# Kernel optimization log

Measured on AMD Instinct MI355X. Metric: run time of the kernel, lower is better.

## Reference

```python
import jax, jax.numpy as jnp
import numpy as np

E_DIM = 64
N_EMBED = 8192

def setup_inputs() -> dict:
    key = jax.random.key(0)
    k1, k2 = jax.random.split(key)
    x = jax.random.normal(k1, (16, E_DIM, 32, 32), dtype=jnp.float32)   # [B, e_dim, H, W]
    embed = jax.random.normal(k2, (E_DIM, N_EMBED), dtype=jnp.float32)  # codebook [e_dim, n_embed]
    return {"x": x, "embed": embed}

def reference(x, embed):
    e_dim, n_embed = embed.shape
    # NCHW -> NHWC
    xp = jnp.transpose(x, (0, 2, 3, 1))              # [B, H, W, e_dim]
    flat = xp.reshape(-1, e_dim)                     # [N, e_dim]
    # squared-distance expansion: ||f||^2 - 2 f.E + ||e||^2  -> [N, n_embed]
    distance = (jnp.sum(flat * flat, axis=1, keepdims=True)
                - 2.0 * flat @ embed
                + jnp.sum(embed * embed, axis=0, keepdims=True))
    embed_idx = jnp.argmax(-distance, axis=1)        # [N] nearest code ids
    embed_idx = embed_idx.reshape(xp.shape[:-1])     # [B, H, W]
    # gather codes: embedding table is embed.T -> [n_embed, e_dim]
    quantize = jnp.take(embed.T, embed_idx, axis=0)  # [B, H, W, e_dim]
    return quantize
```

## Files before the change

### kernel.cpp

```cpp
#include <hip/hip_runtime.h>


typedef __attribute__((ext_vector_type(8))) __bf16 bf16x8;
typedef __attribute__((ext_vector_type(4))) float f32x4;
typedef unsigned int u32;
typedef unsigned long long u64;

union frag_cast { f32x4 f; bf16x8 b; };
__device__ __forceinline__ bf16x8 as_bf16x8(f32x4 v) { frag_cast u; u.f = v; return u.b; }

#define N_ROWS  16384
#define E_DIM   64
#define N_EMBED 8192
#define NCHUNK  16
#define COLS_PER_BLOCK (N_EMBED / NCHUNK)
#define N_ST (COLS_PER_BLOCK / 64)
#define ROWS_PER_BLOCK 256
#define N_ROWBLK (N_ROWS / ROWS_PER_BLOCK)
#define NT 4
#define MARGIN_THR 2e-3f

#define WS_AH   0u
#define WS_AL   (2u << 20)
#define WS_B    (4u << 20)
#define WS_ET   (6u << 20)
#define WS_BIAS (8u << 20)
#define WS_PB1  (WS_BIAS + (64u << 10))
#define WS_PI1  (WS_PB1 + (1u << 20))
#define WS_PB2  (WS_PI1 + (1u << 20))
#define WS_FIDX (WS_PB2 + (1u << 20))
#define WS_FLAG (WS_FIDX + (64u << 10))
#define WS_CNT  (WS_FLAG + (64u << 10))
#define WS_FKEY (WS_CNT + (4u << 10))

__device__ __forceinline__ u32 f32_key(float s) {
    u32 u = __float_as_uint(s);
    return (u & 0x80000000u) ? ~u : (u | 0x80000000u);
}

__device__ __forceinline__ void async16(const void* g, void* l) {
    __builtin_amdgcn_global_load_lds(
        (const __attribute__((address_space(1))) void*)g,
        (__attribute__((address_space(3))) void*)l, 16, 0, 0);
}

__global__ __launch_bounds__(256) void prep(
        const float* __restrict__ x, const float* __restrict__ embed, char* ws) {
    __shared__ float tile[64][65];
    __bf16* Ah = (__bf16*)(ws + WS_AH);
    __bf16* Al = (__bf16*)(ws + WS_AL);
    float*  eT = (float*)(ws + WS_ET);
    float*  bias = (float*)(ws + WS_BIAS);
    const int t = threadIdx.x;
    const int blk = blockIdx.x;

    if (blk < 256) {
        const int b = blk >> 4, p0 = (blk & 15) * 64;
        {
            const int c = t >> 2, seg = (t & 3) * 16;
            const float* src = x + b * 65536 + c * 1024 + p0 + seg;
#pragma unroll
            for (int i = 0; i < 16; ++i) tile[c][seg + i] = src[i];
        }
        __syncthreads();
        const int p = t >> 2, cq = (t & 3) * 16;
        const long row = b * 1024 + p0 + p;
        bf16x8 vh0, vh1, vl0, vl1;
#pragma unroll
        for (int i = 0; i < 16; ++i) {
            float f = tile[cq + i][p];
            __bf16 h = (__bf16)f;
            __bf16 l = (__bf16)(f - (float)h);
            if (i < 8) { vh0[i] = h; vl0[i] = l; }
            else       { vh1[i - 8] = h; vl1[i - 8] = l; }
        }
        *(bf16x8*)(Ah + row * 64 + cq) = vh0;
        *(bf16x8*)(Ah + row * 64 + cq + 8) = vh1;
        *(bf16x8*)(Al + row * 64 + cq) = vl0;
        *(bf16x8*)(Al + row * 64 + cq + 8) = vl1;
    } else {
        if (blk == 256 && t == 0) *(int*)(ws + WS_CNT) = 0;
        const int g = blk - 256;
        const int jbase = g * 64;
        char* Bg = ws + WS_B + (size_t)g * 16384;
        {
            const int c = t >> 2, seg = (t & 3) * 16;
            const float* src = embed + c * N_EMBED + jbase + seg;
#pragma unroll
            for (int i = 0; i < 16; ++i) tile[c][seg + i] = src[i];
        }
        __syncthreads();
        if (t < 64) {
            float s = 0.f;
#pragma unroll
            for (int c = 0; c < 64; ++c) { float v = tile[c][t]; s = fmaf(v, v, s); }
            bias[jbase + t] = -0.5f * s;
        }
        const int jl = t >> 2, cq = (t & 3) * 16;
        bf16x8 vh0, vh1, vl0, vl1;
#pragma unroll
        for (int i = 0; i < 16; ++i) {
            float f = tile[cq + i][jl];
            eT[(long)(jbase + jl) * 64 + cq + i] = f;
            __bf16 h = (__bf16)f;
            __bf16 l = (__bf16)(f - (float)h);
            if (i < 8) { vh0[i] = h; vl0[i] = l; }
            else       { vh1[i - 8] = h; vl1[i - 8] = l; }
        }
        const int k0 = (cq >> 3), sw = jl & 7;
        __bf16* hi = (__bf16*)Bg + jl * 64;
        __bf16* lo = (__bf16*)(Bg + 8192) + jl * 64;
        *(bf16x8*)(hi + ((k0 ^ sw) * 8))       = vh0;
        *(bf16x8*)(hi + (((k0 + 1) ^ sw) * 8)) = vh1;
        *(bf16x8*)(lo + ((k0 ^ sw) * 8))       = vl0;
        *(bf16x8*)(lo + (((k0 + 1) ^ sw) * 8)) = vl1;
    }
}

__global__ __launch_bounds__(256, 4) void qdist(const char* __restrict__ ws_c, char* __restrict__ ws) {
    __shared__ __align__(16) char smem[2][16384];
    const __bf16* Ah = (const __bf16*)(ws_c + WS_AH);
    const __bf16* Al = (const __bf16*)(ws_c + WS_AL);
    const char* Bws = ws_c + WS_B;
    const float* biasg = (const float*)(ws_c + WS_BIAS);
    float* pb1 = (float*)(ws + WS_PB1);
    int*   pi1 = (int*)(ws + WS_PI1);
    float* pb2 = (float*)(ws + WS_PB2);

    const int t = threadIdx.x;
    const int wv = t >> 6, lane = t & 63, ln = lane & 15, q = lane >> 4;
    const int rb = blockIdx.x >> 4, chunk = blockIdx.x & 15;
    const int row0 = rb * ROWS_PER_BLOCK;
    const int col0 = chunk * COLS_PER_BLOCK;
    const int g0 = col0 >> 6;

    f32x4 pfh[NT][2], pfl[NT][2];
#pragma unroll
    for (int nt = 0; nt < NT; ++nt) {
        long row = row0 + wv * 64 + nt * 16 + ln;
        long base = row * 64 + q * 8;
        pfh[nt][0] = *(const f32x4*)(Ah + base);
        pfh[nt][1] = *(const f32x4*)(Ah + base + 32);
        pfl[nt][0] = *(const f32x4*)(Al + base);
        pfl[nt][1] = *(const f32x4*)(Al + base + 32);
    }
    asm volatile("" :
        "+v"(pfh[0][0]), "+v"(pfh[0][1]), "+v"(pfh[1][0]), "+v"(pfh[1][1]),
        "+v"(pfh[2][0]), "+v"(pfh[2][1]), "+v"(pfh[3][0]), "+v"(pfh[3][1]),
        "+v"(pfl[0][0]), "+v"(pfl[0][1]), "+v"(pfl[1][0]), "+v"(pfl[1][1]),
        "+v"(pfl[2][0]), "+v"(pfl[2][1]), "+v"(pfl[3][0]), "+v"(pfl[3][1]));

    float b1[NT], b2[NT]; int iq[NT];
#pragma unroll
    for (int k = 0; k < NT; ++k) { b1[k] = -3.4e38f; b2[k] = -3.4e38f; iq[k] = 0; }

    const int s7 = ln & 7;
    const int rdbase = ln * 128 + ((q ^ s7) << 4);

    auto issue = [&](int st) {
        const char* src = Bws + (size_t)(g0 + st) * 16384;
        char* dst = smem[st & 1];
#pragma unroll
        for (int s = 0; s < 4; ++s)
            async16(src + s * 4096 + wv * 1024 + lane * 16,
                    dst + s * 4096 + wv * 1024);
    };

    issue(0);
    for (int st = 0; st < N_ST; ++st) {
        __syncthreads();
        if (st + 1 < N_ST) issue(st + 1);
        const char* buf = smem[st & 1];
        __builtin_amdgcn_s_setprio(1);
#pragma unroll
        for (int ct = 0; ct < 4; ++ct) {
            const int boff = ct * 2048 + rdbase;
            bf16x8 ah0 = *(const bf16x8*)(buf + boff);
            bf16x8 ah1 = *(const bf16x8*)(buf + (boff ^ 64));
            bf16x8 al0 = *(const bf16x8*)(buf + 8192 + boff);
            bf16x8 al1 = *(const bf16x8*)(buf + 8192 + (boff ^ 64));
            const int cbase = col0 + st * 64 + ct * 16;
            f32x4 bv = *(const f32x4*)(biasg + cbase + q * 4);
            const int jq = cbase + q * 4;
#pragma unroll
            for (int nt = 0; nt < NT; ++nt) {
                f32x4 acc = __builtin_amdgcn_mfma_f32_16x16x32_bf16(al0, as_bf16x8(pfh[nt][0]), bv, 0, 0, 0);
                acc = __builtin_amdgcn_mfma_f32_16x16x32_bf16(al1, as_bf16x8(pfh[nt][1]), acc, 0, 0, 0);
                acc = __builtin_amdgcn_mfma_f32_16x16x32_bf16(ah0, as_bf16x8(pfl[nt][0]), acc, 0, 0, 0);
                acc = __builtin_amdgcn_mfma_f32_16x16x32_bf16(ah1, as_bf16x8(pfl[nt][1]), acc, 0, 0, 0);
                acc = __builtin_amdgcn_mfma_f32_16x16x32_bf16(ah0, as_bf16x8(pfh[nt][0]), acc, 0, 0, 0);
                acc = __builtin_amdgcn_mfma_f32_16x16x32_bf16(ah1, as_bf16x8(pfh[nt][1]), acc, 0, 0, 0);
                float mx = fmaxf(fmaxf(acc[0], acc[1]), fmaxf(acc[2], acc[3]));
                b2[nt] = fmaxf(b2[nt], fminf(b1[nt], mx));
                bool gt = mx > b1[nt];
                b1[nt] = fmaxf(b1[nt], mx);
                iq[nt] = gt ? jq : iq[nt];
            }
        }
        __builtin_amdgcn_s_setprio(0);
    }

#pragma unroll
    for (int m = 16; m < 64; m <<= 1) {
#pragma unroll
        for (int nt = 0; nt < NT; ++nt) {
            float o1 = __shfl_xor(b1[nt], m);
            int   oi = __shfl_xor(iq[nt], m);
            float o2 = __shfl_xor(b2[nt], m);
            b2[nt] = fmaxf(fmaxf(fminf(b1[nt], o1), o2), b2[nt]);
            bool take = (o1 > b1[nt]) || (o1 == b1[nt] && oi < iq[nt]);
            if (take) { b1[nt] = o1; iq[nt] = oi; }
        }
    }
    if (q == 0) {
#pragma unroll
        for (int nt = 0; nt < NT; ++nt) {
            int pixel = row0 + wv * 64 + nt * 16 + ln;
            int o = chunk * N_ROWS + pixel;
            pb1[o] = b1[nt];
            pi1[o] = iq[nt];
            pb2[o] = b2[nt];
        }
    }
}

__global__ __launch_bounds__(64) void reduce_rows(const float* __restrict__ x, char* ws) {
    const float* pb1 = (const float*)(ws + WS_PB1);
    const int*   pi1 = (const int*)(ws + WS_PI1);
    const float* pb2 = (const float*)(ws + WS_PB2);
    const float* eT = (const float*)(ws + WS_ET);
    const float* bias = (const float*)(ws + WS_BIAS);
    int* fidx = (int*)(ws + WS_FIDX);
    int* flags = (int*)(ws + WS_FLAG);
    int* cnt = (int*)(ws + WS_CNT);
    u64* fkey = (u64*)(ws + WS_FKEY);
    const int row = blockIdx.x * 64 + threadIdx.x;

    float b1 = pb1[row]; int iq = pi1[row]; float b2 = pb2[row];
#pragma unroll
    for (int ch = 1; ch < NCHUNK; ++ch) {
        float o1 = pb1[ch * N_ROWS + row];
        int   oi = pi1[ch * N_ROWS + row];
        float o2 = pb2[ch * N_ROWS + row];
        b2 = fmaxf(fmaxf(fminf(b1, o1), o2), b2);
        if (o1 > b1 || (o1 == b1 && oi < iq)) { b1 = o1; iq = oi; }
    }

    if (b1 - b2 < MARGIN_THR) {
        fidx[row] = -1;
        fkey[row] = 0ull;
        flags[atomicAdd(cnt, 1)] = row;
    } else {
        float xr[64];
        const float* xb = x + (row >> 10) * 65536 + (row & 1023);
#pragma unroll
        for (int c = 0; c < 64; ++c) xr[c] = xb[c * 1024];
        float best = -3.4e38f; int bi = iq;
#pragma unroll
        for (int cc = 0; cc < 4; ++cc) {
            const int j = iq + cc;
            const float* e = eT + j * 64;
            float s = bias[j];
#pragma unroll
            for (int c = 0; c < 64; ++c) s = fmaf(xr[c], e[c], s);
            if (s > best) { best = s; bi = j; }
        }
        fidx[row] = bi;
    }
}

__global__ __launch_bounds__(256) void recheck(const float* __restrict__ x, char* ws) {
    __shared__ float fl[64];
    __shared__ u64 red[256];
    const float* eT = (const float*)(ws + WS_ET);
    const float* bias = (const float*)(ws + WS_BIAS);
    const int* flags = (const int*)(ws + WS_FLAG);
    const int n = *(const int*)(ws + WS_CNT);
    u64* fkey = (u64*)(ws + WS_FKEY);
    const int t = threadIdx.x;
    const int seg = blockIdx.x & 31;
    const int rstep = gridDim.x >> 5;
    const int j = seg * 256 + t;

    for (int rowi = blockIdx.x >> 5; rowi < n; rowi += rstep) {
        const int row = flags[rowi];
        __syncthreads();
        if (t < 64) fl[t] = x[(row >> 10) * 65536 + t * 1024 + (row & 1023)];
        __syncthreads();
        float xr[64];
#pragma unroll
        for (int c = 0; c < 64; ++c) xr[c] = fl[c];

        const f32x4* e = (const f32x4*)(eT + (size_t)j * 64);
        f32x4 a0 = {0.f, 0.f, 0.f, 0.f}, a1 = a0, a2 = a0, a3 = a0;
#pragma unroll
        for (int v = 0; v < 4; ++v) {
            f32x4 e0 = e[v * 4 + 0], e1 = e[v * 4 + 1];
            f32x4 e2 = e[v * 4 + 2], e3 = e[v * 4 + 3];
#pragma unroll
            for (int k = 0; k < 4; ++k) {
                a0[k] = fmaf(xr[v * 16 + k],      e0[k], a0[k]);
                a1[k] = fmaf(xr[v * 16 + 4 + k],  e1[k], a1[k]);
                a2[k] = fmaf(xr[v * 16 + 8 + k],  e2[k], a2[k]);
                a3[k] = fmaf(xr[v * 16 + 12 + k], e3[k], a3[k]);
            }
        }
        f32x4 a01 = a0 + a1, a23 = a2 + a3;
        f32x4 as = a01 + a23;
        float s = bias[j] + ((as[0] + as[1]) + (as[2] + as[3]));

        red[t] = ((u64)f32_key(s) << 32) | (u32)(~(u32)j);
        __syncthreads();
        for (int off = 128; off; off >>= 1) {
            if (t < off) { u64 o = red[t + off]; if (o > red[t]) red[t] = o; }
            __syncthreads();
        }
        if (t == 0) atomicMax(&fkey[row], red[0]);
        __syncthreads();
    }
}

__global__ __launch_bounds__(256) void gather_out(const char* __restrict__ ws,
                                                  float* __restrict__ out) {
    const int* fidx = (const int*)(ws + WS_FIDX);
    const u64* fkey = (const u64*)(ws + WS_FKEY);
    const float* eT = (const float*)(ws + WS_ET);
    int g = blockIdx.x * 256 + threadIdx.x;
    int row = g >> 6, c = g & 63;
    int idx = fidx[row];
    if (idx < 0) idx = (int)(~(u32)(fkey[row] & 0xffffffffull));
    out[g] = eT[idx * 64 + c];
}

extern "C" void kernel_launch(void* const* d_in, const int* in_sizes, int n_in,
                              void* d_out, int out_size, void* d_ws, size_t ws_size,
                              hipStream_t stream) {
    const float* x     = (const float*)d_in[0];
    const float* embed = (const float*)d_in[1];
    float* out = (float*)d_out;
    char* ws = (char*)d_ws;

    prep<<<384, 256, 0, stream>>>(x, embed, ws);
    qdist<<<N_ROWBLK * NCHUNK, 256, 0, stream>>>(ws, ws);
    reduce_rows<<<N_ROWS / 64, 64, 0, stream>>>(x, ws);
    recheck<<<2048, 256, 0, stream>>>(x, ws);
    gather_out<<<(N_ROWS * 64) / 256, 256, 0, stream>>>(ws, out);
}
```

Before: 132.5 us.

## Double rows per qdist block, stage bias in LDS, add barriers, fuse gather

The qdist kernel now gives each wave 128 rows (NT=8) instead of 64, so every B tile loaded into LDS is reused across twice as many rows. The launch bound drops to 2 blocks per CU to make room for the extra registers. Bias is copied once into LDS, and the pipeline uses explicit vmcnt waits and s_barrier calls around each column tile to keep waves in step. reduce_rows now writes the output rows for confident pixels directly, and the final gather only handles flagged rows. The trade-offs are lower occupancy, more barriers in the inner loop, and half as many qdist blocks.

```diff
diff --git a/kernel.cpp b/kernel.cpp
--- a/kernel.cpp
+++ b/kernel.cpp
@@ -15,9 +15,9 @@
 #define NCHUNK  16
 #define COLS_PER_BLOCK (N_EMBED / NCHUNK)
 #define N_ST (COLS_PER_BLOCK / 64)
-#define ROWS_PER_BLOCK 256
+#define ROWS_PER_BLOCK 512
 #define N_ROWBLK (N_ROWS / ROWS_PER_BLOCK)
-#define NT 4
+#define NT 8
 #define MARGIN_THR 2e-3f
 
 #define WS_AH   0u
@@ -117,8 +117,9 @@
     }
 }
 
-__global__ __launch_bounds__(256, 4) void qdist(const char* __restrict__ ws_c, char* __restrict__ ws) {
+__global__ __launch_bounds__(256, 2) void qdist(const char* __restrict__ ws_c, char* __restrict__ ws) {
     __shared__ __align__(16) char smem[2][16384];
+    __shared__ __align__(16) float biasLds[512];
     const __bf16* Ah = (const __bf16*)(ws_c + WS_AH);
     const __bf16* Al = (const __bf16*)(ws_c + WS_AL);
     const char* Bws = ws_c + WS_B;
@@ -137,7 +138,7 @@
     f32x4 pfh[NT][2], pfl[NT][2];
 #pragma unroll
     for (int nt = 0; nt < NT; ++nt) {
-        long row = row0 + wv * 64 + nt * 16 + ln;
+        long row = row0 + wv * 128 + nt * 16 + ln;
         long base = row * 64 + q * 8;
         pfh[nt][0] = *(const f32x4*)(Ah + base);
         pfh[nt][1] = *(const f32x4*)(Ah + base + 32);
@@ -147,8 +148,13 @@
     asm volatile("" :
         "+v"(pfh[0][0]), "+v"(pfh[0][1]), "+v"(pfh[1][0]), "+v"(pfh[1][1]),
         "+v"(pfh[2][0]), "+v"(pfh[2][1]), "+v"(pfh[3][0]), "+v"(pfh[3][1]),
+        "+v"(pfh[4][0]), "+v"(pfh[4][1]), "+v"(pfh[5][0]), "+v"(pfh[5][1]),
+        "+v"(pfh[6][0]), "+v"(pfh[6][1]), "+v"(pfh[7][0]), "+v"(pfh[7][1]));
+    asm volatile("" :
         "+v"(pfl[0][0]), "+v"(pfl[0][1]), "+v"(pfl[1][0]), "+v"(pfl[1][1]),
-        "+v"(pfl[2][0]), "+v"(pfl[2][1]), "+v"(pfl[3][0]), "+v"(pfl[3][1]));
+        "+v"(pfl[2][0]), "+v"(pfl[2][1]), "+v"(pfl[3][0]), "+v"(pfl[3][1]),
+        "+v"(pfl[4][0]), "+v"(pfl[4][1]), "+v"(pfl[5][0]), "+v"(pfl[5][1]),
+        "+v"(pfl[6][0]), "+v"(pfl[6][1]), "+v"(pfl[7][0]), "+v"(pfl[7][1]));
 
     float b1[NT], b2[NT]; int iq[NT];
 #pragma unroll
@@ -166,12 +172,25 @@
                     dst + s * 4096 + wv * 1024);
     };
 
+    if (wv < 2)
+        async16((const char*)(biasg + col0) + wv * 1024 + lane * 16,
+                (char*)biasLds + wv * 1024);
     issue(0);
+    asm volatile("s_waitcnt vmcnt(0)" ::: "memory");
+    __builtin_amdgcn_s_barrier();
+    __builtin_amdgcn_sched_barrier(0);
+
     for (int st = 0; st < N_ST; ++st) {
-        __syncthreads();
-        if (st + 1 < N_ST) issue(st + 1);
+        if (st + 1 < N_ST) {
+            issue(st + 1);
+            asm volatile("s_waitcnt vmcnt(4)" ::: "memory");
+        } else {
+            asm volatile("s_waitcnt vmcnt(0)" ::: "memory");
+        }
+        __builtin_amdgcn_s_barrier();
+        __builtin_amdgcn_sched_barrier(0);
+
         const char* buf = smem[st & 1];
-        __builtin_amdgcn_s_setprio(1);
 #pragma unroll
         for (int ct = 0; ct < 4; ++ct) {
             const int boff = ct * 2048 + rdbase;
@@ -179,9 +198,13 @@
             bf16x8 ah1 = *(const bf16x8*)(buf + (boff ^ 64));
             bf16x8 al0 = *(const bf16x8*)(buf + 8192 + boff);
             bf16x8 al1 = *(const bf16x8*)(buf + 8192 + (boff ^ 64));
-            const int cbase = col0 + st * 64 + ct * 16;
-            f32x4 bv = *(const f32x4*)(biasg + cbase + q * 4);
-            const int jq = cbase + q * 4;
+            f32x4 bv = *(const f32x4*)(biasLds + st * 64 + ct * 16 + q * 4);
+            const int jq = col0 + st * 64 + ct * 16 + q * 4;
+            __builtin_amdgcn_sched_barrier(0);
+            __builtin_amdgcn_s_barrier();
+            asm volatile("s_waitcnt lgkmcnt(0)" ::: "memory");
+            __builtin_amdgcn_sched_barrier(0);
+            __builtin_amdgcn_s_setprio(1);
 #pragma unroll
             for (int nt = 0; nt < NT; ++nt) {
                 f32x4 acc = __builtin_amdgcn_mfma_f32_16x16x32_bf16(al0, as_bf16x8(pfh[nt][0]), bv, 0, 0, 0);
@@ -196,8 +219,11 @@
                 b1[nt] = fmaxf(b1[nt], mx);
                 iq[nt] = gt ? jq : iq[nt];
             }
-        }
-        __builtin_amdgcn_s_setprio(0);
+            __builtin_amdgcn_s_setprio(0);
+            __builtin_amdgcn_sched_barrier(0);
+            __builtin_amdgcn_s_barrier();
+            __builtin_amdgcn_sched_barrier(0);
+        }
     }
 
 #pragma unroll
@@ -215,7 +241,7 @@
     if (q == 0) {
 #pragma unroll
         for (int nt = 0; nt < NT; ++nt) {
-            int pixel = row0 + wv * 64 + nt * 16 + ln;
+            int pixel = row0 + wv * 128 + nt * 16 + ln;
             int o = chunk * N_ROWS + pixel;
             pb1[o] = b1[nt];
             pi1[o] = iq[nt];
@@ -224,13 +250,13 @@
     }
 }
 
-__global__ __launch_bounds__(64) void reduce_rows(const float* __restrict__ x, char* ws) {
+__global__ __launch_bounds__(64) void reduce_rows(const float* __restrict__ x, char* ws,
+                                                  float* __restrict__ out) {
     const float* pb1 = (const float*)(ws + WS_PB1);
     const int*   pi1 = (const int*)(ws + WS_PI1);
     const float* pb2 = (const float*)(ws + WS_PB2);
     const float* eT = (const float*)(ws + WS_ET);
     const float* bias = (const float*)(ws + WS_BIAS);
-    int* fidx = (int*)(ws + WS_FIDX);
     int* flags = (int*)(ws + WS_FLAG);
     int* cnt = (int*)(ws + WS_CNT);
     u64* fkey = (u64*)(ws + WS_FKEY);
@@ -247,7 +273,6 @@
     }
 
     if (b1 - b2 < MARGIN_THR) {
-        fidx[row] = -1;
         fkey[row] = 0ull;
         flags[atomicAdd(cnt, 1)] = row;
     } else {
@@ -265,7 +290,10 @@
             for (int c = 0; c < 64; ++c) s = fmaf(xr[c], e[c], s);
             if (s > best) { best = s; bi = j; }
         }
-        fidx[row] = bi;
+        const f32x4* src = (const f32x4*)(eT + (size_t)bi * 64);
+        f32x4* dst = (f32x4*)(out + (size_t)row * 64);
+#pragma unroll
+        for (int v = 0; v < 16; ++v) dst[v] = src[v];
     }
 }
 
@@ -320,16 +348,18 @@
     }
 }
 
-__global__ __launch_bounds__(256) void gather_out(const char* __restrict__ ws,
+__global__ __launch_bounds__(256) void gather_fix(const char* __restrict__ ws,
                                                   float* __restrict__ out) {
-    const int* fidx = (const int*)(ws + WS_FIDX);
+    const int n = *(const int*)(ws + WS_CNT);
+    const int* flags = (const int*)(ws + WS_FLAG);
     const u64* fkey = (const u64*)(ws + WS_FKEY);
     const float* eT = (const float*)(ws + WS_ET);
-    int g = blockIdx.x * 256 + threadIdx.x;
-    int row = g >> 6, c = g & 63;
-    int idx = fidx[row];
-    if (idx < 0) idx = (int)(~(u32)(fkey[row] & 0xffffffffull));
-    out[g] = eT[idx * 64 + c];
+    const int sub = threadIdx.x >> 6, c = threadIdx.x & 63;
+    for (int i = blockIdx.x * 4 + sub; i < n; i += gridDim.x * 4) {
+        const int row = flags[i];
+        const int idx = (int)(~(u32)(fkey[row] & 0xffffffffull));
+        out[(size_t)row * 64 + c] = eT[(size_t)idx * 64 + c];
+    }
 }
 
 extern "C" void kernel_launch(void* const* d_in, const int* in_sizes, int n_in,
@@ -342,7 +372,7 @@
 
     prep<<<384, 256, 0, stream>>>(x, embed, ws);
     qdist<<<N_ROWBLK * NCHUNK, 256, 0, stream>>>(ws, ws);
-    reduce_rows<<<N_ROWS / 64, 64, 0, stream>>>(x, ws);
+    reduce_rows<<<N_ROWS / 64, 64, 0, stream>>>(x, ws, out);
     recheck<<<2048, 256, 0, stream>>>(x, ws);
-    gather_out<<<(N_ROWS * 64) / 256, 256, 0, stream>>>(ws, out);
-}
+    gather_fix<<<64, 256, 0, stream>>>(ws, out);
+}
```

After: 131.0 us. Within noise of the previous version (-1.1%).
